# Performance work log

Hardware: AMD Instinct MI355X
Metric: run time of the kernel (lower is better)

Reference implementation:

```python
import jax, jax.numpy as jnp
import numpy as np

# --- constants (match init_kwargs / input_specs) ---
N_NODES = 32768   # total nodes
N_EDGES = 262144  # total edges (avg degree 8)
B = 512           # number of graphs
D = 64            # node feature / hidden dim (scalar irreps width)
DE = 16           # edge attribute dim
NEXP = 8          # num_experts
K = 2             # top-k


def setup_inputs() -> dict:
    key = jax.random.key(0)
    ks = jax.random.split(key, 20)
    x = jax.random.normal(ks[0], (N_NODES, D), dtype=jnp.float32)
    edge_src = jax.random.randint(ks[1], (N_EDGES,), 0, N_NODES, dtype=jnp.int32)
    edge_dst = jax.random.randint(ks[2], (N_EDGES,), 0, N_NODES, dtype=jnp.int32)
    edge_attr = jax.random.normal(ks[3], (N_EDGES, DE), dtype=jnp.float32)
    # sorted graph ids, every graph non-empty (64 nodes each)
    batch = jnp.repeat(jnp.arange(B, dtype=jnp.int32), N_NODES // B)
    s = 1.0 / np.sqrt(D)
    se = 1.0 / np.sqrt(DE)
    # embedding GNN params
    emb_We = jax.random.normal(ks[4], (DE, D), dtype=jnp.float32) * se
    emb_W1 = jax.random.normal(ks[5], (D, D), dtype=jnp.float32) * s
    emb_W2 = jax.random.normal(ks[6], (D, D), dtype=jnp.float32) * s
    emb_b = jnp.zeros((D,), dtype=jnp.float32)
    # gating network
    Wg = jax.random.normal(ks[7], (D, NEXP), dtype=jnp.float32) * s
    bg = jnp.zeros((NEXP,), dtype=jnp.float32)
    # stacked expert params [NEXP, ...]
    ex_We = jax.random.normal(ks[8], (NEXP, DE, D), dtype=jnp.float32) * se
    ex_W1 = jax.random.normal(ks[9], (NEXP, D, D), dtype=jnp.float32) * s
    ex_W2 = jax.random.normal(ks[10], (NEXP, D, D), dtype=jnp.float32) * s
    ex_b = jnp.zeros((NEXP, D), dtype=jnp.float32)
    ex_Wout = jax.random.normal(ks[11], (NEXP, D, 1), dtype=jnp.float32) * s
    ex_bout = jnp.zeros((NEXP, 1), dtype=jnp.float32)
    return {
        "x": x, "edge_attr": edge_attr,
        "emb_We": emb_We, "emb_W1": emb_W1, "emb_W2": emb_W2, "emb_b": emb_b,
        "Wg": Wg, "bg": bg,
        "ex_We": ex_We, "ex_W1": ex_W1, "ex_W2": ex_W2, "ex_b": ex_b,
        "ex_Wout": ex_Wout, "ex_bout": ex_bout,
        "edge_src": edge_src, "edge_dst": edge_dst, "batch": batch,
    }


def _gnn_embed(x, edge_attr, We, W1, W2, b, src, dst, batch):
    # edge-gated messages: gather x[src], modulate by projected edge attrs, scatter to dst
    msg = x[src] * (edge_attr @ We)                          # [E, D]
    agg = jax.ops.segment_sum(msg, dst, num_segments=N_NODES)  # [N, D]
    h = jax.nn.relu(x @ W1 + agg @ W2 + b)                   # [N, D]
    # mean pooling per graph
    gsum = jax.ops.segment_sum(h, batch, num_segments=B)      # [B, D]
    cnt = jax.ops.segment_sum(jnp.ones((N_NODES, 1), h.dtype), batch, num_segments=B)
    return gsum / jnp.maximum(cnt, 1.0)                      # [B, D]


def _expert(x, edge_attr, We, W1, W2, b, Wout, bout, src, dst, batch):
    emb = _gnn_embed(x, edge_attr, We, W1, W2, b, src, dst, batch)
    return emb @ Wout + bout                                  # [B, 1]


def reference(x, edge_attr, emb_We, emb_W1, emb_W2, emb_b, Wg, bg,
              ex_We, ex_W1, ex_W2, ex_b, ex_Wout, ex_bout,
              edge_src, edge_dst, batch):
    # 1) graph embeddings via embedding GNN
    graph_emb = _gnn_embed(x, edge_attr, emb_We, emb_W1, emb_W2, emb_b,
                           edge_src, edge_dst, batch)          # [B, D]
    # 2) gating: softmax over experts, top-k, renormalize
    routing_weights = jax.nn.softmax(graph_emb @ Wg + bg, axis=1)  # [B, NEXP]
    top_k_weights, top_k_indices = jax.lax.top_k(routing_weights, K)
    norm_top_k = jax.nn.softmax(top_k_weights, axis=1)             # [B, K]
    # 3) dispatch: run every expert on the full batch (vectorized equivalent of
    #    the per-expert masked sub-batch loop), then gather routed outputs
    expert_outs = jax.vmap(
        lambda We, W1, W2, b, Wo, bo: _expert(
            x, edge_attr, We, W1, W2, b, Wo, bo, edge_src, edge_dst, batch)
    )(ex_We, ex_W1, ex_W2, ex_b, ex_Wout, ex_bout)             # [NEXP, B, 1]
    per_graph = expert_outs[:, :, 0].T                         # [B, NEXP]
    gathered = jnp.take_along_axis(per_graph, top_k_indices, axis=1)  # [B, K]
    # 4) weighted combine
    final_output = jnp.sum(gathered * norm_top_k, axis=1, keepdims=True)  # [B, 1]
    return final_output, routing_weights
```

## Files before the change

kernel.cpp:

```cpp
#include <hip/hip_runtime.h>

#define N_NODES 32768
#define N_EDGES 262144
#define NB      512
#define D       64
#define DE      16
#define NEXP    8

typedef __attribute__((ext_vector_type(8))) short  short8v;
typedef __attribute__((ext_vector_type(4))) float  floatx4;

static __device__ __forceinline__ unsigned short f2bf(float f) {
  unsigned int u = __float_as_uint(f);
  u += 0x7FFFu + ((u >> 16) & 1u);
  return (unsigned short)(u >> 16);
}


__global__ void hist_kernel(const int* __restrict__ dst, int* __restrict__ counts) {
  int i = blockIdx.x * blockDim.x + threadIdx.x;
  if (i < N_EDGES) atomicAdd(&counts[dst[i]], 1);
}

__global__ void scan1_kernel(const int* __restrict__ counts, int* __restrict__ offsets,
                             int* __restrict__ bsums) {
  __shared__ int sm[256];
  int t = threadIdx.x, i = blockIdx.x * 256 + t;
  int v = counts[i];
  sm[t] = v;
  __syncthreads();
  for (int off = 1; off < 256; off <<= 1) {
    int u = (t >= off) ? sm[t - off] : 0;
    __syncthreads();
    sm[t] += u;
    __syncthreads();
  }
  offsets[i] = sm[t] - v;
  if (t == 255) bsums[blockIdx.x] = sm[255];
}

__global__ void scan2_kernel(int* __restrict__ bsums) {
  __shared__ int sm[128];
  int t = threadIdx.x;
  int v = bsums[t];
  sm[t] = v;
  __syncthreads();
  for (int off = 1; off < 128; off <<= 1) {
    int u = (t >= off) ? sm[t - off] : 0;
    __syncthreads();
    sm[t] += u;
    __syncthreads();
  }
  bsums[t] = sm[t] - v;
}

__global__ void scan3_kernel(int* __restrict__ offsets, const int* __restrict__ bsums,
                             int* __restrict__ cursor) {
  int i = blockIdx.x * 256 + threadIdx.x;
  int v = offsets[i] + bsums[blockIdx.x];
  offsets[i] = v;
  cursor[i]  = v;
  if (i == 0) offsets[N_NODES] = N_EDGES;
}

__global__ void scatter_kernel(const int* __restrict__ dst, const int* __restrict__ src,
                               const float4* __restrict__ ea4, int* __restrict__ cursor,
                               int* __restrict__ sorted_src, float4* __restrict__ sea4) {
  int i = blockIdx.x * blockDim.x + threadIdx.x;
  if (i < N_EDGES) {
    int p = atomicAdd(&cursor[dst[i]], 1);
    sorted_src[p] = src[i];
    float4 a = ea4[(size_t)i * 4 + 0];
    float4 b = ea4[(size_t)i * 4 + 1];
    float4 c = ea4[(size_t)i * 4 + 2];
    float4 d = ea4[(size_t)i * 4 + 3];
    sea4[(size_t)p * 4 + 0] = a;
    sea4[(size_t)p * 4 + 1] = b;
    sea4[(size_t)p * 4 + 2] = c;
    sea4[(size_t)p * 4 + 3] = d;
  }
}

__global__ void wpack_kernel(const float* __restrict__ ex_W1, const float* __restrict__ ex_W2,
                             unsigned short* __restrict__ wpk) {
  int idx = blockIdx.x * 256 + threadIdx.x;
  int je  = idx >> 13;
  int rem = idx & 8191;
  int mat = rem >> 12;
  int cd  = rem & 4095;
  int col = cd >> 6, k = cd & 63;
  const float* W = mat ? ex_W2 : ex_W1;
  wpk[idx] = f2bf(W[je * 4096 + k * 64 + col]);
}


__global__ __launch_bounds__(256) void agg_kernel(
    const float* __restrict__ x, const int* __restrict__ sorted_src,
    const float4* __restrict__ sea4, const int* __restrict__ offsets,
    const float* __restrict__ emb_We, const float* __restrict__ ex_We,
    float* __restrict__ agg0, unsigned short* __restrict__ aggb) {
  int lane = threadIdx.x & 63;
  int n = blockIdx.x * 4 + (threadIdx.x >> 6);
  int st = offsets[n], en = offsets[n + 1];
  float t[DE];
#pragma unroll
  for (int k = 0; k < DE; ++k) t[k] = 0.f;

  for (int base = st; base < en; base += 8) {
    int m = en - base;
    if (m > 8) m = 8;
    int sj[8];
#pragma unroll
    for (int j = 0; j < 8; ++j) sj[j] = sorted_src[base + ((j < m) ? j : 0)];
    float xv[8];
#pragma unroll
    for (int j = 0; j < 8; ++j) xv[j] = x[(size_t)sj[j] * D + lane];
#pragma unroll
    for (int j = 0; j < 8; ++j) {
      if (j < m) {
        const float4* ep = sea4 + ((size_t)(base + j) << 2);
        float4 e0 = ep[0], e1 = ep[1], e2 = ep[2], e3 = ep[3];
        float xvj = xv[j];
        t[0]  += xvj * e0.x; t[1]  += xvj * e0.y; t[2]  += xvj * e0.z; t[3]  += xvj * e0.w;
        t[4]  += xvj * e1.x; t[5]  += xvj * e1.y; t[6]  += xvj * e1.z; t[7]  += xvj * e1.w;
        t[8]  += xvj * e2.x; t[9]  += xvj * e2.y; t[10] += xvj * e2.z; t[11] += xvj * e2.w;
        t[12] += xvj * e3.x; t[13] += xvj * e3.y; t[14] += xvj * e3.z; t[15] += xvj * e3.w;
      }
    }
  }
  {
    float a = 0.f;
#pragma unroll
    for (int k = 0; k < DE; ++k) a += t[k] * emb_We[k * D + lane];
    agg0[(size_t)n * D + lane] = a;
  }
  for (int je = 0; je < NEXP; ++je) {
    const float* We = ex_We + (size_t)je * DE * D;
    float a = 0.f;
#pragma unroll
    for (int k = 0; k < DE; ++k) a += t[k] * We[k * D + lane];
    aggb[((size_t)je * N_NODES + n) * D + lane] = f2bf(a);
  }
}


__global__ __launch_bounds__(256) void gnn0_kernel(
    const float* __restrict__ x, const float* __restrict__ agg0,
    const float* __restrict__ W1, const float* __restrict__ W2,
    const float* __restrict__ bvv, float* __restrict__ graph_emb) {
  __shared__ __align__(16) float w1s[D * D];
  __shared__ __align__(16) float w2s[D * D];
  __shared__ __align__(16) float xs[D * D];
  __shared__ __align__(16) float as2[D * D];
  int b = blockIdx.x;
  int t = threadIdx.x;
  const float4* w1src = (const float4*)W1;
  const float4* w2src = (const float4*)W2;
  const float4* xsrc  = (const float4*)(x    + (size_t)b * D * D);
  const float4* asrc  = (const float4*)(agg0 + (size_t)b * D * D);
#pragma unroll
  for (int r = 0; r < 4; ++r) {
    ((float4*)w1s)[t + r * 256] = w1src[t + r * 256];
    ((float4*)w2s)[t + r * 256] = w2src[t + r * 256];
    ((float4*)xs)[t + r * 256]  = xsrc[t + r * 256];
    ((float4*)as2)[t + r * 256] = asrc[t + r * 256];
  }
  int w = t >> 6, lane = t & 63;
  float bias = bvv[lane];
  __syncthreads();
  float pool = 0.f;
#pragma unroll
  for (int q = 0; q < 4; ++q) {
    int n0 = w * 16 + q * 4;
    float a0 = bias, a1 = bias, a2 = bias, a3 = bias;
#pragma unroll 4
    for (int c4 = 0; c4 < 16; ++c4) {
      float4 x0 = *(const float4*)&xs[(n0 + 0) * D + c4 * 4];
      float4 x1 = *(const float4*)&xs[(n0 + 1) * D + c4 * 4];
      float4 x2 = *(const float4*)&xs[(n0 + 2) * D + c4 * 4];
      float4 x3 = *(const float4*)&xs[(n0 + 3) * D + c4 * 4];
      float4 g0 = *(const float4*)&as2[(n0 + 0) * D + c4 * 4];
      float4 g1 = *(const float4*)&as2[(n0 + 1) * D + c4 * 4];
      float4 g2 = *(const float4*)&as2[(n0 + 2) * D + c4 * 4];
      float4 g3 = *(const float4*)&as2[(n0 + 3) * D + c4 * 4];
      float w10 = w1s[(c4 * 4 + 0) * D + lane];
      float w11 = w1s[(c4 * 4 + 1) * D + lane];
      float w12 = w1s[(c4 * 4 + 2) * D + lane];
      float w13 = w1s[(c4 * 4 + 3) * D + lane];
      float w20 = w2s[(c4 * 4 + 0) * D + lane];
      float w21 = w2s[(c4 * 4 + 1) * D + lane];
      float w22 = w2s[(c4 * 4 + 2) * D + lane];
      float w23 = w2s[(c4 * 4 + 3) * D + lane];
      a0 += x0.x * w10 + x0.y * w11 + x0.z * w12 + x0.w * w13
          + g0.x * w20 + g0.y * w21 + g0.z * w22 + g0.w * w23;
      a1 += x1.x * w10 + x1.y * w11 + x1.z * w12 + x1.w * w13
          + g1.x * w20 + g1.y * w21 + g1.z * w22 + g1.w * w23;
      a2 += x2.x * w10 + x2.y * w11 + x2.z * w12 + x2.w * w13
          + g2.x * w20 + g2.y * w21 + g2.z * w22 + g2.w * w23;
      a3 += x3.x * w10 + x3.y * w11 + x3.z * w12 + x3.w * w13
          + g3.x * w20 + g3.y * w21 + g3.z * w22 + g3.w * w23;
    }
    pool += fmaxf(a0, 0.f) + fmaxf(a1, 0.f) + fmaxf(a2, 0.f) + fmaxf(a3, 0.f);
  }
  __syncthreads();
  xs[w * D + lane] = pool;
  __syncthreads();
  if (w == 0) {
    float s = xs[lane] + xs[D + lane] + xs[2 * D + lane] + xs[3 * D + lane];
    graph_emb[b * D + lane] = s * (1.f / 64.f);
  }
}


__global__ __launch_bounds__(512) void gnn_mfma_kernel(
    const float* __restrict__ x, const unsigned short* __restrict__ aggb,
    const unsigned short* __restrict__ wpk,
    const float* __restrict__ ex_b, const float* __restrict__ ex_Wout,
    const float* __restrict__ ex_bout, float* __restrict__ per_graph) {
  __shared__ __align__(16) short xls[4096];
  int g = blockIdx.x;
  int t = threadIdx.x;
  {
    const float4* xp = (const float4*)(x + (size_t)g * 4096 + (size_t)t * 8);
    float4 va = xp[0], vb = xp[1];
    short8v pk;
    pk[0] = (short)f2bf(va.x); pk[1] = (short)f2bf(va.y);
    pk[2] = (short)f2bf(va.z); pk[3] = (short)f2bf(va.w);
    pk[4] = (short)f2bf(vb.x); pk[5] = (short)f2bf(vb.y);
    pk[6] = (short)f2bf(vb.z); pk[7] = (short)f2bf(vb.w);
    int row = t >> 3, slot = t & 7;
    *(short8v*)((char*)xls + (((row << 3) + (slot ^ (row & 7))) << 4)) = pk;
  }
  __syncthreads();

  int wv = t >> 6;
  int je = wv;
  int lane = t & 63;
  int r = lane & 15, q = lane >> 4;

  const short* Ab = (const short*)(aggb + ((size_t)je * N_NODES + (size_t)g * D) * D);
  const short* B1 = (const short*)(wpk + (size_t)je * 2 * 4096);
  const short* B2 = B1 + 4096;

  floatx4 acc[4][4];
#pragma unroll
  for (int i = 0; i < 4; ++i)
#pragma unroll
    for (int j = 0; j < 4; ++j) acc[i][j] = (floatx4){0.f, 0.f, 0.f, 0.f};

#pragma unroll
  for (int kk = 0; kk < 2; ++kk) {
    int ko = kk * 32 + q * 8;
    short8v af[4], bf[4];
#pragma unroll
    for (int rt = 0; rt < 4; ++rt) {
      int row = rt * 16 + r;
      int slot = kk * 4 + q;
      af[rt] = *(const short8v*)((char*)xls + (((row << 3) + (slot ^ (row & 7))) << 4));
    }
#pragma unroll
    for (int ct = 0; ct < 4; ++ct) bf[ct] = *(const short8v*)(B1 + (ct * 16 + r) * D + ko);
#pragma unroll
    for (int rt = 0; rt < 4; ++rt)
#pragma unroll
      for (int ct = 0; ct < 4; ++ct)
        acc[rt][ct] = __builtin_amdgcn_mfma_f32_16x16x32_bf16(af[rt], bf[ct], acc[rt][ct], 0, 0, 0);
  }
#pragma unroll
  for (int kk = 0; kk < 2; ++kk) {
    int ko = kk * 32 + q * 8;
    short8v af[4], bf[4];
#pragma unroll
    for (int rt = 0; rt < 4; ++rt) af[rt] = *(const short8v*)(Ab + (rt * 16 + r) * D + ko);
#pragma unroll
    for (int ct = 0; ct < 4; ++ct) bf[ct] = *(const short8v*)(B2 + (ct * 16 + r) * D + ko);
#pragma unroll
    for (int rt = 0; rt < 4; ++rt)
#pragma unroll
      for (int ct = 0; ct < 4; ++ct)
        acc[rt][ct] = __builtin_amdgcn_mfma_f32_16x16x32_bf16(af[rt], bf[ct], acc[rt][ct], 0, 0, 0);
  }

  float o = 0.f;
#pragma unroll
  for (int ct = 0; ct < 4; ++ct) {
    float bcol = ex_b[je * D + ct * 16 + r];
    float s = 0.f;
#pragma unroll
    for (int rt = 0; rt < 4; ++rt)
#pragma unroll
      for (int rg = 0; rg < 4; ++rg) s += fmaxf(acc[rt][ct][rg] + bcol, 0.f);
    s += __shfl_xor(s, 16);
    s += __shfl_xor(s, 32);
    o += s * ex_Wout[je * D + ct * 16 + r];
  }
#pragma unroll
  for (int off = 8; off >= 1; off >>= 1) o += __shfl_xor(o, off);
  if (lane == 0) per_graph[g * NEXP + je] = o * (1.f / 64.f) + ex_bout[je];
}


__global__ void gate_kernel(const float* __restrict__ graph_emb, const float* __restrict__ Wg,
                            const float* __restrict__ bg, const float* __restrict__ per_graph,
                            float* __restrict__ out) {
  __shared__ float es[D];
  __shared__ float lg[NEXP];
  int b = blockIdx.x, lane = threadIdx.x;
  es[lane] = graph_emb[b * D + lane];
  __syncthreads();
  if (lane < NEXP) {
    float v = bg[lane];
    for (int d = 0; d < D; ++d) v += es[d] * Wg[d * NEXP + lane];
    lg[lane] = v;
  }
  __syncthreads();
  float l[NEXP];
  float mx = -1e30f;
#pragma unroll
  for (int e = 0; e < NEXP; ++e) { l[e] = lg[e]; mx = fmaxf(mx, l[e]); }
  float p[NEXP];
  float sum = 0.f;
#pragma unroll
  for (int e = 0; e < NEXP; ++e) { p[e] = expf(l[e] - mx); sum += p[e]; }
  float inv = 1.f / sum;
#pragma unroll
  for (int e = 0; e < NEXP; ++e) p[e] *= inv;
  if (lane < NEXP) out[NB + b * NEXP + lane] = p[lane];
  if (lane == 0) {
    int i1 = -1; float v1 = -1e30f;
#pragma unroll
    for (int e = 0; e < NEXP; ++e) if (p[e] > v1) { v1 = p[e]; i1 = e; }
    int i2 = -1; float v2 = -1e30f;
#pragma unroll
    for (int e = 0; e < NEXP; ++e) if (e != i1 && p[e] > v2) { v2 = p[e]; i2 = e; }
    float rr = expf(v2 - v1);
    float n1 = 1.f / (1.f + rr);
    float n2 = rr / (1.f + rr);
    out[b] = n1 * per_graph[b * NEXP + i1] + n2 * per_graph[b * NEXP + i2];
  }
}


extern "C" void kernel_launch(void* const* d_in, const int* in_sizes, int n_in,
                              void* d_out, int out_size, void* d_ws, size_t ws_size,
                              hipStream_t stream) {
  const float* x         = (const float*)d_in[0];
  const float* edge_attr = (const float*)d_in[1];
  const float* emb_We    = (const float*)d_in[2];
  const float* emb_W1    = (const float*)d_in[3];
  const float* emb_W2    = (const float*)d_in[4];
  const float* emb_b     = (const float*)d_in[5];
  const float* Wg        = (const float*)d_in[6];
  const float* bg        = (const float*)d_in[7];
  const float* ex_We     = (const float*)d_in[8];
  const float* ex_W1     = (const float*)d_in[9];
  const float* ex_W2     = (const float*)d_in[10];
  const float* ex_b      = (const float*)d_in[11];
  const float* ex_Wout   = (const float*)d_in[12];
  const float* ex_bout   = (const float*)d_in[13];
  const int* edge_src    = (const int*)d_in[14];
  const int* edge_dst    = (const int*)d_in[15];

  char* p = (char*)d_ws;
  auto alloc = [&](size_t bytes) {
    char* q = p;
    p += (bytes + 255) & ~(size_t)255;
    return q;
  };
  int*   counts     = (int*)alloc((size_t)N_NODES * 4);
  int*   offsets    = (int*)alloc((size_t)(N_NODES + 1) * 4);
  int*   cursor     = (int*)alloc((size_t)N_NODES * 4);
  int*   bsums      = (int*)alloc(128 * 4);
  int*   sorted_src = (int*)alloc((size_t)N_EDGES * 4);
  float* sorted_ea  = (float*)alloc((size_t)N_EDGES * DE * 4);
  float* agg0       = (float*)alloc((size_t)N_NODES * D * 4);
  unsigned short* aggb = (unsigned short*)alloc((size_t)NEXP * N_NODES * D * 2);
  unsigned short* wpk  = (unsigned short*)alloc((size_t)NEXP * 2 * D * D * 2);
  float* graph_emb  = (float*)alloc((size_t)NB * D * 4);
  float* per_graph  = (float*)alloc((size_t)NB * NEXP * 4);

  hipMemsetAsync(counts, 0, (size_t)N_NODES * 4, stream);
  hist_kernel<<<N_EDGES / 256, 256, 0, stream>>>(edge_dst, counts);
  scan1_kernel<<<N_NODES / 256, 256, 0, stream>>>(counts, offsets, bsums);
  scan2_kernel<<<1, 128, 0, stream>>>(bsums);
  scan3_kernel<<<N_NODES / 256, 256, 0, stream>>>(offsets, bsums, cursor);
  scatter_kernel<<<N_EDGES / 256, 256, 0, stream>>>(edge_dst, edge_src,
                                                    (const float4*)edge_attr, cursor,
                                                    sorted_src, (float4*)sorted_ea);
  wpack_kernel<<<(NEXP * 2 * D * D) / 256, 256, 0, stream>>>(ex_W1, ex_W2, wpk);
  agg_kernel<<<N_NODES / 4, 256, 0, stream>>>(x, sorted_src, (const float4*)sorted_ea,
                                              offsets, emb_We, ex_We, agg0, aggb);
  gnn0_kernel<<<NB, 256, 0, stream>>>(x, agg0, emb_W1, emb_W2, emb_b, graph_emb);
  gnn_mfma_kernel<<<NB, 512, 0, stream>>>(x, aggb, wpk, ex_b, ex_Wout, ex_bout, per_graph);
  gate_kernel<<<NB, 64, 0, stream>>>(graph_emb, Wg, bg, per_graph, (float*)d_out);
}
```

Measured before the change: 246.3 us.

## Fuse weight packing into scatter, gate into expert kernel, restructure aggregation

Weight packing is folded into the scatter kernel and the gating/top-k combine is folded into the tail of the MFMA expert kernel, removing two launches and the per_graph round-trip through global memory. The aggregation kernel now stages all nine edge-projection matrices in shared memory, and each 512-thread block processes 32 nodes (4 per wave) with 4-edge batches whose edge-attribute loads are issued before the x gathers. This trades a smaller unroll and a large LDS footprint (36KB per block) for less repeated global weight traffic and fewer launches.

```diff
diff --git a/kernel.cpp b/kernel.cpp
--- a/kernel.cpp
+++ b/kernel.cpp
@@ -65,7 +65,9 @@
 
 __global__ void scatter_kernel(const int* __restrict__ dst, const int* __restrict__ src,
                                const float4* __restrict__ ea4, int* __restrict__ cursor,
-                               int* __restrict__ sorted_src, float4* __restrict__ sea4) {
+                               int* __restrict__ sorted_src, float4* __restrict__ sea4,
+                               const float* __restrict__ ex_W1, const float* __restrict__ ex_W2,
+                               unsigned short* __restrict__ wpk) {
   int i = blockIdx.x * blockDim.x + threadIdx.x;
   if (i < N_EDGES) {
     int p = atomicAdd(&cursor[dst[i]], 1);
@@ -79,67 +81,86 @@
     sea4[(size_t)p * 4 + 2] = c;
     sea4[(size_t)p * 4 + 3] = d;
   }
-}
-
-__global__ void wpack_kernel(const float* __restrict__ ex_W1, const float* __restrict__ ex_W2,
-                             unsigned short* __restrict__ wpk) {
-  int idx = blockIdx.x * 256 + threadIdx.x;
-  int je  = idx >> 13;
-  int rem = idx & 8191;
-  int mat = rem >> 12;
-  int cd  = rem & 4095;
-  int col = cd >> 6, k = cd & 63;
-  const float* W = mat ? ex_W2 : ex_W1;
-  wpk[idx] = f2bf(W[je * 4096 + k * 64 + col]);
-}
-
-
-__global__ __launch_bounds__(256) void agg_kernel(
+  if (i < NEXP * 2 * D * D) {
+    int je  = i >> 13;
+    int rem = i & 8191;
+    int mat = rem >> 12;
+    int cd  = rem & 4095;
+    int col = cd >> 6, k = cd & 63;
+    const float* W = mat ? ex_W2 : ex_W1;
+    wpk[i] = f2bf(W[je * 4096 + k * 64 + col]);
+  }
+}
+
+
+__global__ __launch_bounds__(512, 4) void agg_kernel(
     const float* __restrict__ x, const int* __restrict__ sorted_src,
     const float4* __restrict__ sea4, const int* __restrict__ offsets,
     const float* __restrict__ emb_We, const float* __restrict__ ex_We,
     float* __restrict__ agg0, unsigned short* __restrict__ aggb) {
-  int lane = threadIdx.x & 63;
-  int n = blockIdx.x * 4 + (threadIdx.x >> 6);
-  int st = offsets[n], en = offsets[n + 1];
-  float t[DE];
-#pragma unroll
-  for (int k = 0; k < DE; ++k) t[k] = 0.f;
-
-  for (int base = st; base < en; base += 8) {
-    int m = en - base;
-    if (m > 8) m = 8;
-    int sj[8];
-#pragma unroll
-    for (int j = 0; j < 8; ++j) sj[j] = sorted_src[base + ((j < m) ? j : 0)];
-    float xv[8];
-#pragma unroll
-    for (int j = 0; j < 8; ++j) xv[j] = x[(size_t)sj[j] * D + lane];
-#pragma unroll
-    for (int j = 0; j < 8; ++j) {
-      if (j < m) {
-        const float4* ep = sea4 + ((size_t)(base + j) << 2);
-        float4 e0 = ep[0], e1 = ep[1], e2 = ep[2], e3 = ep[3];
-        float xvj = xv[j];
-        t[0]  += xvj * e0.x; t[1]  += xvj * e0.y; t[2]  += xvj * e0.z; t[3]  += xvj * e0.w;
-        t[4]  += xvj * e1.x; t[5]  += xvj * e1.y; t[6]  += xvj * e1.z; t[7]  += xvj * e1.w;
-        t[8]  += xvj * e2.x; t[9]  += xvj * e2.y; t[10] += xvj * e2.z; t[11] += xvj * e2.w;
-        t[12] += xvj * e3.x; t[13] += xvj * e3.y; t[14] += xvj * e3.z; t[15] += xvj * e3.w;
+  __shared__ float weS[9 * DE * D];
+  int t = threadIdx.x;
+  for (int i = t; i < 9 * DE * D; i += 512) {
+    int j = i >> 10;
+    int rem = i & 1023;
+    weS[i] = (j == 0) ? emb_We[rem] : ex_We[(size_t)(j - 1) * 1024 + rem];
+  }
+  __syncthreads();
+  int wv = t >> 6, lane = t & 63;
+
+  for (int it = 0; it < 4; ++it) {
+    int n = blockIdx.x * 32 + wv * 4 + it;
+    int st = offsets[n], en = offsets[n + 1];
+    float tk[DE];
+#pragma unroll
+    for (int k = 0; k < DE; ++k) tk[k] = 0.f;
+
+    for (int base = st; base < en; base += 4) {
+      int m = en - base;
+      if (m > 4) m = 4;
+      int idx[4], sj[4];
+      float xv[4];
+      float4 e0[4], e1[4], e2[4], e3[4];
+#pragma unroll
+      for (int j = 0; j < 4; ++j) idx[j] = base + ((j < m) ? j : 0);
+#pragma unroll
+      for (int j = 0; j < 4; ++j) sj[j] = sorted_src[idx[j]];
+#pragma unroll
+      for (int j = 0; j < 4; ++j) {
+        const float4* ep = sea4 + ((size_t)idx[j] << 2);
+        e0[j] = ep[0]; e1[j] = ep[1]; e2[j] = ep[2]; e3[j] = ep[3];
       }
-    }
-  }
-  {
-    float a = 0.f;
-#pragma unroll
-    for (int k = 0; k < DE; ++k) a += t[k] * emb_We[k * D + lane];
-    agg0[(size_t)n * D + lane] = a;
-  }
-  for (int je = 0; je < NEXP; ++je) {
-    const float* We = ex_We + (size_t)je * DE * D;
-    float a = 0.f;
-#pragma unroll
-    for (int k = 0; k < DE; ++k) a += t[k] * We[k * D + lane];
-    aggb[((size_t)je * N_NODES + n) * D + lane] = f2bf(a);
+#pragma unroll
+      for (int j = 0; j < 4; ++j) xv[j] = x[(size_t)sj[j] * D + lane];
+#pragma unroll
+      for (int j = 0; j < 4; ++j) {
+        if (j < m) {
+          float xvj = xv[j];
+          tk[0]  += xvj * e0[j].x; tk[1]  += xvj * e0[j].y;
+          tk[2]  += xvj * e0[j].z; tk[3]  += xvj * e0[j].w;
+          tk[4]  += xvj * e1[j].x; tk[5]  += xvj * e1[j].y;
+          tk[6]  += xvj * e1[j].z; tk[7]  += xvj * e1[j].w;
+          tk[8]  += xvj * e2[j].x; tk[9]  += xvj * e2[j].y;
+          tk[10] += xvj * e2[j].z; tk[11] += xvj * e2[j].w;
+          tk[12] += xvj * e3[j].x; tk[13] += xvj * e3[j].y;
+          tk[14] += xvj * e3[j].z; tk[15] += xvj * e3[j].w;
+        }
+      }
+    }
+    {
+      float a = 0.f;
+#pragma unroll
+      for (int k = 0; k < DE; ++k) a += tk[k] * weS[k * 64 + lane];
+      agg0[(size_t)n * D + lane] = a;
+    }
+#pragma unroll
+    for (int je = 0; je < NEXP; ++je) {
+      const float* w = &weS[(je + 1) * 1024];
+      float a = 0.f;
+#pragma unroll
+      for (int k = 0; k < DE; ++k) a += tk[k] * w[k * 64 + lane];
+      aggb[((size_t)je * N_NODES + n) * D + lane] = f2bf(a);
+    }
   }
 }
 
@@ -216,8 +237,12 @@
     const float* __restrict__ x, const unsigned short* __restrict__ aggb,
     const unsigned short* __restrict__ wpk,
     const float* __restrict__ ex_b, const float* __restrict__ ex_Wout,
-    const float* __restrict__ ex_bout, float* __restrict__ per_graph) {
+    const float* __restrict__ ex_bout,
+    const float* __restrict__ graph_emb, const float* __restrict__ Wg,
+    const float* __restrict__ bg, float* __restrict__ out) {
   __shared__ __align__(16) short xls[4096];
+  __shared__ float pg[NEXP];
+  __shared__ float lg[NEXP];
   int g = blockIdx.x;
   int t = threadIdx.x;
   {
@@ -233,8 +258,7 @@
   }
   __syncthreads();
 
-  int wv = t >> 6;
-  int je = wv;
+  int je = t >> 6;
   int lane = t & 63;
   int r = lane & 15, q = lane >> 4;
 
@@ -296,47 +320,43 @@
   }
 #pragma unroll
   for (int off = 8; off >= 1; off >>= 1) o += __shfl_xor(o, off);
-  if (lane == 0) per_graph[g * NEXP + je] = o * (1.f / 64.f) + ex_bout[je];
-}
-
-
-__global__ void gate_kernel(const float* __restrict__ graph_emb, const float* __restrict__ Wg,
-                            const float* __restrict__ bg, const float* __restrict__ per_graph,
-                            float* __restrict__ out) {
-  __shared__ float es[D];
-  __shared__ float lg[NEXP];
-  int b = blockIdx.x, lane = threadIdx.x;
-  es[lane] = graph_emb[b * D + lane];
-  __syncthreads();
-  if (lane < NEXP) {
-    float v = bg[lane];
-    for (int d = 0; d < D; ++d) v += es[d] * Wg[d * NEXP + lane];
-    lg[lane] = v;
-  }
-  __syncthreads();
-  float l[NEXP];
-  float mx = -1e30f;
-#pragma unroll
-  for (int e = 0; e < NEXP; ++e) { l[e] = lg[e]; mx = fmaxf(mx, l[e]); }
-  float p[NEXP];
-  float sum = 0.f;
-#pragma unroll
-  for (int e = 0; e < NEXP; ++e) { p[e] = expf(l[e] - mx); sum += p[e]; }
-  float inv = 1.f / sum;
-#pragma unroll
-  for (int e = 0; e < NEXP; ++e) p[e] *= inv;
-  if (lane < NEXP) out[NB + b * NEXP + lane] = p[lane];
-  if (lane == 0) {
-    int i1 = -1; float v1 = -1e30f;
-#pragma unroll
-    for (int e = 0; e < NEXP; ++e) if (p[e] > v1) { v1 = p[e]; i1 = e; }
-    int i2 = -1; float v2 = -1e30f;
-#pragma unroll
-    for (int e = 0; e < NEXP; ++e) if (e != i1 && p[e] > v2) { v2 = p[e]; i2 = e; }
-    float rr = expf(v2 - v1);
-    float n1 = 1.f / (1.f + rr);
-    float n2 = rr / (1.f + rr);
-    out[b] = n1 * per_graph[b * NEXP + i1] + n2 * per_graph[b * NEXP + i2];
+  if (lane == 0) pg[je] = o * (1.f / 64.f) + ex_bout[je];
+  __syncthreads();
+
+  float* es = (float*)xls;
+  if (t < 64) es[t] = graph_emb[g * D + t];
+  __syncthreads();
+  if (t < NEXP) {
+    float v = bg[t];
+    for (int d = 0; d < D; ++d) v += es[d] * Wg[d * NEXP + t];
+    lg[t] = v;
+  }
+  __syncthreads();
+  if (t < NEXP) {
+    float l[NEXP];
+    float mx = -1e30f;
+#pragma unroll
+    for (int e = 0; e < NEXP; ++e) { l[e] = lg[e]; mx = fmaxf(mx, l[e]); }
+    float p[NEXP];
+    float sum = 0.f;
+#pragma unroll
+    for (int e = 0; e < NEXP; ++e) { p[e] = expf(l[e] - mx); sum += p[e]; }
+    float inv = 1.f / sum;
+#pragma unroll
+    for (int e = 0; e < NEXP; ++e) p[e] *= inv;
+    out[NB + g * NEXP + t] = p[t];
+    if (t == 0) {
+      int i1 = -1; float v1 = -1e30f;
+#pragma unroll
+      for (int e = 0; e < NEXP; ++e) if (p[e] > v1) { v1 = p[e]; i1 = e; }
+      int i2 = -1; float v2 = -1e30f;
+#pragma unroll
+      for (int e = 0; e < NEXP; ++e) if (e != i1 && p[e] > v2) { v2 = p[e]; i2 = e; }
+      float rr = expf(v2 - v1);
+      float n1 = 1.f / (1.f + rr);
+      float n2 = rr / (1.f + rr);
+      out[g] = n1 * pg[i1] + n2 * pg[i2];
+    }
   }
 }
 
@@ -377,7 +397,6 @@
   unsigned short* aggb = (unsigned short*)alloc((size_t)NEXP * N_NODES * D * 2);
   unsigned short* wpk  = (unsigned short*)alloc((size_t)NEXP * 2 * D * D * 2);
   float* graph_emb  = (float*)alloc((size_t)NB * D * 4);
-  float* per_graph  = (float*)alloc((size_t)NB * NEXP * 4);
 
   hipMemsetAsync(counts, 0, (size_t)N_NODES * 4, stream);
   hist_kernel<<<N_EDGES / 256, 256, 0, stream>>>(edge_dst, counts);
@@ -386,11 +405,11 @@
   scan3_kernel<<<N_NODES / 256, 256, 0, stream>>>(offsets, bsums, cursor);
   scatter_kernel<<<N_EDGES / 256, 256, 0, stream>>>(edge_dst, edge_src,
                                                     (const float4*)edge_attr, cursor,
-                                                    sorted_src, (float4*)sorted_ea);
-  wpack_kernel<<<(NEXP * 2 * D * D) / 256, 256, 0, stream>>>(ex_W1, ex_W2, wpk);
-  agg_kernel<<<N_NODES / 4, 256, 0, stream>>>(x, sorted_src, (const float4*)sorted_ea,
-                                              offsets, emb_We, ex_We, agg0, aggb);
+                                                    sorted_src, (float4*)sorted_ea,
+                                                    ex_W1, ex_W2, wpk);
+  agg_kernel<<<N_NODES / 32, 512, 0, stream>>>(x, sorted_src, (const float4*)sorted_ea,
+                                               offsets, emb_We, ex_We, agg0, aggb);
   gnn0_kernel<<<NB, 256, 0, stream>>>(x, agg0, emb_W1, emb_W2, emb_b, graph_emb);
-  gnn_mfma_kernel<<<NB, 512, 0, stream>>>(x, aggb, wpk, ex_b, ex_Wout, ex_bout, per_graph);
-  gate_kernel<<<NB, 64, 0, stream>>>(graph_emb, Wg, bg, per_graph, (float*)d_out);
-}
+  gnn_mfma_kernel<<<NB, 512, 0, stream>>>(x, aggb, wpk, ex_b, ex_Wout, ex_bout,
+                                          graph_emb, Wg, bg, (float*)d_out);
+}
```

Measured after the change: 426.4 us. +73.1%, slower.
